# Performance work log

Hardware: AMD Instinct MI355X
Metric: run time of the kernel (lower is better)

## Reference

```python
import jax, jax.numpy as jnp
import numpy as np

B, C, Hf, Wf, HM, P = 64, 2048, 16, 16, 256, 10  # P = num_parts, NP = graph nodes
NP = P - 1
EPS = 1e-5  # BatchNorm eps

def bn_eval(x, g, b, rm, rv):
    return (x - rm) * jax.lax.rsqrt(rv + EPS) * g + b

def setup_inputs() -> dict:
    key = jax.random.key(0)
    ks = jax.random.split(key, 6)
    return {
        "x_global": jax.random.normal(ks[0], (B, C, Hf, Wf), jnp.float32),
        "x_gcn": jax.random.normal(ks[1], (B, C, Hf, Wf), jnp.float32),
        "mask": jax.random.randint(ks[2], (B, 1, HM, HM), 0, P, jnp.int32),
        "adj": jax.random.uniform(ks[3], (B, NP, NP), jnp.float32),
        "W1": jax.random.normal(ks[4], (C, C), jnp.float32) * 0.02,
        "b1": jnp.zeros((C,), jnp.float32),
        "g1": jnp.ones((NP * C,), jnp.float32), "be1": jnp.zeros((NP * C,), jnp.float32),
        "rm1": jnp.zeros((NP * C,), jnp.float32), "rv1": jnp.ones((NP * C,), jnp.float32),
        "W2": jax.random.normal(ks[5], (C, C), jnp.float32) * 0.02,
        "b2": jnp.zeros((C,), jnp.float32),
        "g2": jnp.ones((NP * C,), jnp.float32), "be2": jnp.zeros((NP * C,), jnp.float32),
        "rm2": jnp.zeros((NP * C,), jnp.float32), "rv2": jnp.ones((NP * C,), jnp.float32),
        "gb_g": jnp.ones((C,), jnp.float32), "gb_b": jnp.zeros((C,), jnp.float32),
        "gb_rm": jnp.zeros((C,), jnp.float32), "gb_rv": jnp.ones((C,), jnp.float32),
        "gn_g": jnp.ones((C,), jnp.float32), "gn_b": jnp.zeros((C,), jnp.float32),
        "gn_rm": jnp.zeros((C,), jnp.float32), "gn_rv": jnp.ones((C,), jnp.float32),
    }

def gc_layer(x, adj, Wt, bias, g, be, rm, rv):
    # GraphConvolution: matmul -> bmm(adj) -> bias -> BN over flattened (B, NP*C)
    s = jnp.einsum('bpc,cd->bpd', x, Wt)
    o = jnp.einsum('bpq,bqd->bpd', adj, s) + bias
    flat = o.reshape(o.shape[0], -1)
    return bn_eval(flat, g, be, rm, rv).reshape(o.shape)

def reference(x_global, x_gcn, mask, adj, W1, b1, g1, be1, rm1, rv1,
              W2, b2, g2, be2, rm2, rv2, gb_g, gb_b, gb_rm, gb_rv,
              gn_g, gn_b, gn_rm, gn_rv):
    # --- global branch: GAP + bottleneck BN (eval) ---
    feat_global = x_global.mean(axis=(2, 3))                      # (B, C)
    bnfeat_global = bn_eval(feat_global, gb_g, gb_b, gb_rm, gb_rv)

    # --- nearest-neighbor downsample of mask to feature-map size ---
    stride = HM // Hf
    mr = mask[:, 0, ::stride, ::stride]                           # (B, h, w)

    # one-hot part masks for classes 1..P-1: (B, h, w, NP)
    onehot = (mr[..., None] == jnp.arange(1, P)).astype(jnp.float32)
    counts = onehot.sum(axis=(1, 2))                              # (B, NP)

    # deterministic part dropout: drop the first present part per image
    drop = jnp.argmax(counts > 0, axis=1) + 1                     # (B,)
    keep = (mr != drop[:, None, None]).astype(jnp.float32)        # (B, h, w)
    x_self = x_gcn * keep[:, None, :, :]

    # segment mean pooling per part: (B, NP, C)
    denom = (counts + 1e-8)[..., None]
    mask_feat = jnp.einsum('bchw,bhwp->bpc', x_gcn, onehot) / denom
    self_feat = jnp.einsum('bchw,bhwp->bpc', x_self, onehot) / denom

    def gcn(x):
        x1 = jax.nn.relu(gc_layer(x, adj, W1, b1, g1, be1, rm1, rv1))
        x2 = jax.nn.relu(gc_layer(x1, adj, W2, b2, g2, be2, rm2, rv2))
        return x2.mean(axis=1), x2.reshape(x2.shape[0], -1)

    feat_gcn, feat_gcn_cat = gcn(mask_feat)
    feat_self, feat_self_cat = gcn(self_feat)
    bnfeat_gcn = bn_eval(feat_gcn, gn_g, gn_b, gn_rm, gn_rv)
    bnfeat_self = bn_eval(feat_self, gn_g, gn_b, gn_rm, gn_rv)

    # concatenate eval-mode outputs into one array: (B, 3*C + 2*NP*C)
    return jnp.concatenate([bnfeat_global, bnfeat_gcn, bnfeat_self,
                            feat_gcn_cat, feat_self_cat], axis=1)
```

## Files before the change

kernel.cpp:

```cpp
#include <hip/hip_runtime.h>
#include <cstdint>
#include <cstddef>

#define EPSV 1e-5f

typedef __bf16 bf16x8 __attribute__((ext_vector_type(8)));
typedef float f32x4 __attribute__((ext_vector_type(4)));

__device__ __forceinline__ unsigned short f2bf(float f) {
  unsigned int u = __float_as_uint(f);
  u += 0x7FFFu + ((u >> 16) & 1u);
  return (unsigned short)(u >> 16);
}

__device__ __forceinline__ void async_copy16(const void* src, void* dst_lds) {
  __builtin_amdgcn_global_load_lds(
      (const __attribute__((address_space(1))) void*)src,
      (__attribute__((address_space(3))) void*)dst_lds, 16, 0, 0);
}

__global__ __launch_bounds__(256) void kmean(
    const float* __restrict__ x, const float* __restrict__ g,
    const float* __restrict__ bb, const float* __restrict__ rm,
    const float* __restrict__ rv, float* __restrict__ out) {
  int gw = blockIdx.x * 4 + (threadIdx.x >> 6);
  int lane = threadIdx.x & 63;
  float4 v = ((const float4*)(x + (size_t)gw * 256))[lane];
  float s = v.x + v.y + v.z + v.w;
#pragma unroll
  for (int o = 32; o > 0; o >>= 1) s += __shfl_xor(s, o, 64);
  if (lane == 0) {
    int b = gw >> 11, c = gw & 2047;
    float m = s * (1.f / 256.f);
    out[(size_t)b * 43008 + c] =
        (m - rm[c]) / sqrtf(rv[c] + EPSV) * g[c] + bb[c];
  }
}

__global__ __launch_bounds__(256) void kmask(
    const int* __restrict__ mask, int* __restrict__ partid,
    float* __restrict__ invden, int* __restrict__ dropm1) {
  int b = blockIdx.x;
  int t = threadIdx.x;
  int h = t >> 4, w = t & 15;
  int m = mask[(size_t)b * 65536 + h * 4096 + w * 16];
  partid[b * 256 + t] = m;
  __shared__ int cnt[10];
  if (t < 10) cnt[t] = 0;
  __syncthreads();
  atomicAdd(&cnt[m], 1);
  __syncthreads();
  if (t == 0) {
    int dp = 0;
    for (int p = 8; p >= 0; p--)
      if (cnt[p + 1] > 0) dp = p;
    dropm1[b] = dp;
  }
  if (t < 9) invden[b * 9 + t] = 1.f / ((float)cnt[t + 1] + 1e-8f);
}

__global__ __launch_bounds__(256) void kpool(
    const float* __restrict__ x, const int* __restrict__ partid,
    const float* __restrict__ invden, const int* __restrict__ dropm1,
    unsigned short* __restrict__ Abuf) {
  int gw = blockIdx.x * 4 + (threadIdx.x >> 6);
  int lane = threadIdx.x & 63;
  int b = gw >> 11, c = gw & 2047;
  int4 pid = ((const int4*)(partid + b * 256))[lane];
  float4 v = ((const float4*)(x + (size_t)gw * 256))[lane];
  float acc[9];
#pragma unroll
  for (int p = 0; p < 9; p++) acc[p] = 0.f;
#pragma unroll
  for (int p = 0; p < 9; p++) {
    acc[p] += (pid.x == p + 1) ? v.x : 0.f;
    acc[p] += (pid.y == p + 1) ? v.y : 0.f;
    acc[p] += (pid.z == p + 1) ? v.z : 0.f;
    acc[p] += (pid.w == p + 1) ? v.w : 0.f;
  }
#pragma unroll
  for (int p = 0; p < 9; p++) {
    float s = acc[p];
#pragma unroll
    for (int o = 32; o > 0; o >>= 1) s += __shfl_xor(s, o, 64);
    acc[p] = s;
  }
  if (lane == 0) {
    int dm1 = dropm1[b];
#pragma unroll
    for (int p = 0; p < 9; p++) {
      float val = acc[p] * invden[b * 9 + p];
      unsigned short h = f2bf(val);
      Abuf[(size_t)(b * 9 + p) * 2048 + c] = h;
      Abuf[(size_t)((64 + b) * 9 + p) * 2048 + c] =
          (p == dm1) ? (unsigned short)0 : h;
    }
  }
}

__global__ __launch_bounds__(256) void ktranspose(
    const float* __restrict__ W, unsigned short* __restrict__ Wt) {
  __shared__ float tile[32][33];
  int tx = threadIdx.x & 31;
  int ty = threadIdx.x >> 5;
  int k0 = blockIdx.y * 32;
  int n0 = blockIdx.x * 32;
#pragma unroll
  for (int i = 0; i < 32; i += 8)
    tile[ty + i][tx] = W[(size_t)(k0 + ty + i) * 2048 + n0 + tx];
  __syncthreads();
#pragma unroll
  for (int i = 0; i < 32; i += 8)
    Wt[(size_t)(n0 + ty + i) * 2048 + k0 + tx] = f2bf(tile[tx][ty + i]);
}

#define GK 2048
__global__ __launch_bounds__(256) void gemm_bf16(
    const unsigned short* __restrict__ A, const unsigned short* __restrict__ Bt,
    float* __restrict__ S) {
  __shared__ unsigned short As[128 * 32];
  __shared__ unsigned short Bs[128 * 32];
  const int tid = threadIdx.x;
  const int lane = tid & 63;
  const int wave = tid >> 6;
  const int wm = (wave >> 1) << 6;
  const int wn = (wave & 1) << 6;
  const int quad = lane >> 4;
  const int l16 = lane & 15;
  const int by = blockIdx.y;
  const int bx = blockIdx.x;

  const unsigned short* Ag = A + (size_t)by * 128 * GK;
  const unsigned short* Bg = Bt + (size_t)bx * 128 * GK;

  f32x4 acc[4][4];
#pragma unroll
  for (int i = 0; i < 4; i++)
#pragma unroll
    for (int j = 0; j < 4; j++) acc[i][j] = (f32x4){0.f, 0.f, 0.f, 0.f};

  const int seg0 = tid, seg1 = tid + 256;
  const int r0 = seg0 >> 2, c0 = (seg0 & 3) * 8;
  const int r1 = seg1 >> 2, c1 = (seg1 & 3) * 8;

  for (int kk = 0; kk < GK; kk += 32) {
    __syncthreads();
    async_copy16(Ag + (size_t)r0 * GK + kk + c0, &As[seg0 * 8]);
    async_copy16(Ag + (size_t)r1 * GK + kk + c1, &As[seg1 * 8]);
    async_copy16(Bg + (size_t)r0 * GK + kk + c0, &Bs[seg0 * 8]);
    async_copy16(Bg + (size_t)r1 * GK + kk + c1, &Bs[seg1 * 8]);
    asm volatile("s_waitcnt vmcnt(0)" ::: "memory");
    __syncthreads();

    bf16x8 af[4], bfr[4];
#pragma unroll
    for (int i = 0; i < 4; i++)
      af[i] = *(const bf16x8*)&As[(wm + i * 16 + l16) * 32 + quad * 8];
#pragma unroll
    for (int j = 0; j < 4; j++)
      bfr[j] = *(const bf16x8*)&Bs[(wn + j * 16 + l16) * 32 + quad * 8];
#pragma unroll
    for (int i = 0; i < 4; i++)
#pragma unroll
      for (int j = 0; j < 4; j++)
        acc[i][j] = __builtin_amdgcn_mfma_f32_16x16x32_bf16(af[i], bfr[j],
                                                            acc[i][j], 0, 0, 0);
  }

#pragma unroll
  for (int i = 0; i < 4; i++)
#pragma unroll
    for (int j = 0; j < 4; j++)
#pragma unroll
      for (int r = 0; r < 4; r++) {
        int m = by * 128 + wm + i * 16 + quad * 4 + r;
        int n = bx * 128 + wn + j * 16 + l16;
        S[(size_t)m * 2048 + n] = acc[i][j][r];
      }
}

__global__ __launch_bounds__(256) void epi_mid(
    const float* __restrict__ S, const float* __restrict__ adj,
    const float* __restrict__ bias, const float* __restrict__ g,
    const float* __restrict__ be, const float* __restrict__ rm,
    const float* __restrict__ rv, unsigned short* __restrict__ Aout) {
  int idx = blockIdx.x * 256 + threadIdx.x;
  int d = idx & 2047;
  int bb = idx >> 11;
  int b = bb & 63;
  float s[9];
#pragma unroll
  for (int q = 0; q < 9; q++) s[q] = S[(size_t)(bb * 9 + q) * 2048 + d];
#pragma unroll
  for (int p = 0; p < 9; p++) {
    float o = bias[d];
#pragma unroll
    for (int q = 0; q < 9; q++) o += adj[b * 81 + p * 9 + q] * s[q];
    int f = p * 2048 + d;
    float v = (o - rm[f]) / sqrtf(rv[f] + EPSV) * g[f] + be[f];
    v = fmaxf(v, 0.f);
    Aout[(size_t)(bb * 9 + p) * 2048 + d] = f2bf(v);
  }
}

__global__ __launch_bounds__(256) void epi_final(
    const float* __restrict__ S, const float* __restrict__ adj,
    const float* __restrict__ bias, const float* __restrict__ g,
    const float* __restrict__ be, const float* __restrict__ rm,
    const float* __restrict__ rv, const float* __restrict__ gn_g,
    const float* __restrict__ gn_b, const float* __restrict__ gn_rm,
    const float* __restrict__ gn_rv, float* __restrict__ out) {
  int idx = blockIdx.x * 256 + threadIdx.x;
  int d = idx & 2047;
  int bb = idx >> 11;
  int b = bb & 63;
  bool selfb = bb >= 64;
  float s[9];
#pragma unroll
  for (int q = 0; q < 9; q++) s[q] = S[(size_t)(bb * 9 + q) * 2048 + d];
  float* orow = out + (size_t)b * 43008;
  size_t catbase = selfb ? 24576 : 6144;
  float mean = 0.f;
#pragma unroll
  for (int p = 0; p < 9; p++) {
    float o = bias[d];
#pragma unroll
    for (int q = 0; q < 9; q++) o += adj[b * 81 + p * 9 + q] * s[q];
    int f = p * 2048 + d;
    float v = (o - rm[f]) / sqrtf(rv[f] + EPSV) * g[f] + be[f];
    v = fmaxf(v, 0.f);
    mean += v;
    orow[catbase + f] = v;
  }
  mean *= (1.f / 9.f);
  orow[(selfb ? 4096 : 2048) + d] =
      (mean - gn_rm[d]) / sqrtf(gn_rv[d] + EPSV) * gn_g[d] + gn_b[d];
}

extern "C" void kernel_launch(void* const* d_in, const int* in_sizes, int n_in,
                              void* d_out, int out_size, void* d_ws,
                              size_t ws_size, hipStream_t stream) {
  const float* x_global = (const float*)d_in[0];
  const float* x_gcn = (const float*)d_in[1];
  const int* mask = (const int*)d_in[2];
  const float* adj = (const float*)d_in[3];
  const float* W1 = (const float*)d_in[4];
  const float* b1 = (const float*)d_in[5];
  const float* g1 = (const float*)d_in[6];
  const float* be1 = (const float*)d_in[7];
  const float* rm1 = (const float*)d_in[8];
  const float* rv1 = (const float*)d_in[9];
  const float* W2 = (const float*)d_in[10];
  const float* b2 = (const float*)d_in[11];
  const float* g2 = (const float*)d_in[12];
  const float* be2 = (const float*)d_in[13];
  const float* rm2 = (const float*)d_in[14];
  const float* rv2 = (const float*)d_in[15];
  const float* gb_g = (const float*)d_in[16];
  const float* gb_b = (const float*)d_in[17];
  const float* gb_rm = (const float*)d_in[18];
  const float* gb_rv = (const float*)d_in[19];
  const float* gn_g = (const float*)d_in[20];
  const float* gn_b = (const float*)d_in[21];
  const float* gn_rm = (const float*)d_in[22];
  const float* gn_rv = (const float*)d_in[23];
  float* out = (float*)d_out;

  char* ws = (char*)d_ws;
  int* partid = (int*)(ws);
  float* invden = (float*)(ws + 65536);
  int* dropm1 = (int*)(ws + 67840);
  unsigned short* Abuf = (unsigned short*)(ws + 131072);
  unsigned short* Wt1 = (unsigned short*)(ws + 131072 + 4718592);
  unsigned short* Wt2 =
      (unsigned short*)(ws + 131072 + 4718592 + 8388608);
  float* S = (float*)(ws + 131072 + 4718592 + 2 * 8388608);

  ktranspose<<<dim3(64, 64), 256, 0, stream>>>(W1, Wt1);
  ktranspose<<<dim3(64, 64), 256, 0, stream>>>(W2, Wt2);
  kmean<<<32768, 256, 0, stream>>>(x_global, gb_g, gb_b, gb_rm, gb_rv, out);
  kmask<<<64, 256, 0, stream>>>(mask, partid, invden, dropm1);
  kpool<<<32768, 256, 0, stream>>>(x_gcn, partid, invden, dropm1, Abuf);
  gemm_bf16<<<dim3(16, 9), 256, 0, stream>>>(Abuf, Wt1, S);
  epi_mid<<<1024, 256, 0, stream>>>(S, adj, b1, g1, be1, rm1, rv1, Abuf);
  gemm_bf16<<<dim3(16, 9), 256, 0, stream>>>(Abuf, Wt2, S);
  epi_final<<<1024, 256, 0, stream>>>(S, adj, b2, g2, be2, rm2, rv2, gn_g,
                                      gn_b, gn_rm, gn_rv, out);
}
```

Before: 504.0 us.

## Use MFMA for part pooling, split-K the GCN GEMMs, merge weight transposes

Part pooling now runs as a bf16 MFMA matmul. Each block turns 64 channels of x into bf16 in LDS and multiplies them by a one-hot part matrix, replacing the per-channel wave shuffle reductions across 32768 blocks. The two 1152x2048x2048 GEMMs use a split-K of 2 to double the grid from 144 blocks. The epilogues sum the two partial result buffers. The two weight-transpose launches become one launch. The trade-offs are rounding x to bf16 before the reduction instead of after, an extra S buffer of workspace plus the epilogue reads for it, and the launch overhead of the larger grid.

```diff
diff --git a/kernel.cpp b/kernel.cpp
--- a/kernel.cpp
+++ b/kernel.cpp
@@ -59,47 +59,71 @@
   if (t < 9) invden[b * 9 + t] = 1.f / ((float)cnt[t + 1] + 1e-8f);
 }
 
-__global__ __launch_bounds__(256) void kpool(
+__global__ __launch_bounds__(256) void kpool_mfma(
     const float* __restrict__ x, const int* __restrict__ partid,
     const float* __restrict__ invden, const int* __restrict__ dropm1,
     unsigned short* __restrict__ Abuf) {
-  int gw = blockIdx.x * 4 + (threadIdx.x >> 6);
-  int lane = threadIdx.x & 63;
-  int b = gw >> 11, c = gw & 2047;
-  int4 pid = ((const int4*)(partid + b * 256))[lane];
-  float4 v = ((const float4*)(x + (size_t)gw * 256))[lane];
-  float acc[9];
-#pragma unroll
-  for (int p = 0; p < 9; p++) acc[p] = 0.f;
-#pragma unroll
-  for (int p = 0; p < 9; p++) {
-    acc[p] += (pid.x == p + 1) ? v.x : 0.f;
-    acc[p] += (pid.y == p + 1) ? v.y : 0.f;
-    acc[p] += (pid.z == p + 1) ? v.z : 0.f;
-    acc[p] += (pid.w == p + 1) ? v.w : 0.f;
-  }
-#pragma unroll
-  for (int p = 0; p < 9; p++) {
-    float s = acc[p];
-#pragma unroll
-    for (int o = 32; o > 0; o >>= 1) s += __shfl_xor(s, o, 64);
-    acc[p] = s;
-  }
-  if (lane == 0) {
+  __shared__ unsigned short As[64 * 264];
+  __shared__ unsigned short Bs[16 * 264];
+  __shared__ int pid[256];
+  const int t = threadIdx.x;
+  const int b = blockIdx.y;
+  const int c0 = blockIdx.x * 64;
+
+  pid[t] = partid[b * 256 + t];
+
+  const float4* xg = (const float4*)(x + ((size_t)(b * 2048 + c0)) * 256);
+#pragma unroll
+  for (int it = 0; it < 16; it++) {
+    int idx = t + it * 256;
+    float4 v = xg[idx];
+    int row = idx >> 6, sc = (idx & 63) * 4;
+    ushort4 h;
+    h.x = f2bf(v.x); h.y = f2bf(v.y); h.z = f2bf(v.z); h.w = f2bf(v.w);
+    *(ushort4*)&As[row * 264 + sc] = h;
+  }
+  __syncthreads();
+  {
+    int p = t >> 4, s0 = (t & 15) * 16;
+#pragma unroll
+    for (int j = 0; j < 16; j++)
+      Bs[p * 264 + s0 + j] =
+          (pid[s0 + j] == p + 1) ? (unsigned short)0x3F80 : (unsigned short)0;
+  }
+  __syncthreads();
+
+  const int wave = t >> 6;
+  const int l16 = t & 15;
+  const int quad = (t & 63) >> 4;
+  f32x4 acc = (f32x4){0.f, 0.f, 0.f, 0.f};
+#pragma unroll
+  for (int ks = 0; ks < 8; ks++) {
+    bf16x8 a = *(const bf16x8*)&As[(wave * 16 + l16) * 264 + ks * 32 + quad * 8];
+    bf16x8 bf = *(const bf16x8*)&Bs[l16 * 264 + ks * 32 + quad * 8];
+    acc = __builtin_amdgcn_mfma_f32_16x16x32_bf16(a, bf, acc, 0, 0, 0);
+  }
+
+  if (l16 < 9) {
+    int p = l16;
+    float inv = invden[b * 9 + p];
     int dm1 = dropm1[b];
-#pragma unroll
-    for (int p = 0; p < 9; p++) {
-      float val = acc[p] * invden[b * 9 + p];
-      unsigned short h = f2bf(val);
-      Abuf[(size_t)(b * 9 + p) * 2048 + c] = h;
-      Abuf[(size_t)((64 + b) * 9 + p) * 2048 + c] =
-          (p == dm1) ? (unsigned short)0 : h;
-    }
+    int cbase = c0 + wave * 16 + quad * 4;
+    ushort4 hm;
+    hm.x = f2bf(acc[0] * inv);
+    hm.y = f2bf(acc[1] * inv);
+    hm.z = f2bf(acc[2] * inv);
+    hm.w = f2bf(acc[3] * inv);
+    ushort4 hs = (p == dm1) ? (ushort4){0, 0, 0, 0} : hm;
+    *(ushort4*)&Abuf[(size_t)(b * 9 + p) * 2048 + cbase] = hm;
+    *(ushort4*)&Abuf[(size_t)((64 + b) * 9 + p) * 2048 + cbase] = hs;
   }
 }
 
 __global__ __launch_bounds__(256) void ktranspose(
-    const float* __restrict__ W, unsigned short* __restrict__ Wt) {
+    const float* __restrict__ W1, const float* __restrict__ W2,
+    unsigned short* __restrict__ Wt1, unsigned short* __restrict__ Wt2) {
+  const float* W = blockIdx.z ? W2 : W1;
+  unsigned short* Wt = blockIdx.z ? Wt2 : Wt1;
   __shared__ float tile[32][33];
   int tx = threadIdx.x & 31;
   int ty = threadIdx.x >> 5;
@@ -129,9 +153,11 @@
   const int l16 = lane & 15;
   const int by = blockIdx.y;
   const int bx = blockIdx.x;
+  const int kz = blockIdx.z;
 
   const unsigned short* Ag = A + (size_t)by * 128 * GK;
   const unsigned short* Bg = Bt + (size_t)bx * 128 * GK;
+  S += (size_t)kz * 1152 * 2048;
 
   f32x4 acc[4][4];
 #pragma unroll
@@ -143,7 +169,8 @@
   const int r0 = seg0 >> 2, c0 = (seg0 & 3) * 8;
   const int r1 = seg1 >> 2, c1 = (seg1 & 3) * 8;
 
-  for (int kk = 0; kk < GK; kk += 32) {
+  const int kbeg = kz * (GK / 2), kend = kbeg + (GK / 2);
+  for (int kk = kbeg; kk < kend; kk += 32) {
     __syncthreads();
     async_copy16(Ag + (size_t)r0 * GK + kk + c0, &As[seg0 * 8]);
     async_copy16(Ag + (size_t)r1 * GK + kk + c1, &As[seg1 * 8]);
@@ -180,17 +207,21 @@
 }
 
 __global__ __launch_bounds__(256) void epi_mid(
-    const float* __restrict__ S, const float* __restrict__ adj,
-    const float* __restrict__ bias, const float* __restrict__ g,
-    const float* __restrict__ be, const float* __restrict__ rm,
-    const float* __restrict__ rv, unsigned short* __restrict__ Aout) {
+    const float* __restrict__ S0, const float* __restrict__ S1,
+    const float* __restrict__ adj, const float* __restrict__ bias,
+    const float* __restrict__ g, const float* __restrict__ be,
+    const float* __restrict__ rm, const float* __restrict__ rv,
+    unsigned short* __restrict__ Aout) {
   int idx = blockIdx.x * 256 + threadIdx.x;
   int d = idx & 2047;
   int bb = idx >> 11;
   int b = bb & 63;
   float s[9];
 #pragma unroll
-  for (int q = 0; q < 9; q++) s[q] = S[(size_t)(bb * 9 + q) * 2048 + d];
+  for (int q = 0; q < 9; q++) {
+    size_t off = (size_t)(bb * 9 + q) * 2048 + d;
+    s[q] = S0[off] + S1[off];
+  }
 #pragma unroll
   for (int p = 0; p < 9; p++) {
     float o = bias[d];
@@ -204,12 +235,13 @@
 }
 
 __global__ __launch_bounds__(256) void epi_final(
-    const float* __restrict__ S, const float* __restrict__ adj,
-    const float* __restrict__ bias, const float* __restrict__ g,
-    const float* __restrict__ be, const float* __restrict__ rm,
-    const float* __restrict__ rv, const float* __restrict__ gn_g,
-    const float* __restrict__ gn_b, const float* __restrict__ gn_rm,
-    const float* __restrict__ gn_rv, float* __restrict__ out) {
+    const float* __restrict__ S0, const float* __restrict__ S1,
+    const float* __restrict__ adj, const float* __restrict__ bias,
+    const float* __restrict__ g, const float* __restrict__ be,
+    const float* __restrict__ rm, const float* __restrict__ rv,
+    const float* __restrict__ gn_g, const float* __restrict__ gn_b,
+    const float* __restrict__ gn_rm, const float* __restrict__ gn_rv,
+    float* __restrict__ out) {
   int idx = blockIdx.x * 256 + threadIdx.x;
   int d = idx & 2047;
   int bb = idx >> 11;
@@ -217,7 +249,10 @@
   bool selfb = bb >= 64;
   float s[9];
 #pragma unroll
-  for (int q = 0; q < 9; q++) s[q] = S[(size_t)(bb * 9 + q) * 2048 + d];
+  for (int q = 0; q < 9; q++) {
+    size_t off = (size_t)(bb * 9 + q) * 2048 + d;
+    s[q] = S0[off] + S1[off];
+  }
   float* orow = out + (size_t)b * 43008;
   size_t catbase = selfb ? 24576 : 6144;
   float mean = 0.f;
@@ -274,16 +309,17 @@
   unsigned short* Wt1 = (unsigned short*)(ws + 131072 + 4718592);
   unsigned short* Wt2 =
       (unsigned short*)(ws + 131072 + 4718592 + 8388608);
-  float* S = (float*)(ws + 131072 + 4718592 + 2 * 8388608);
-
-  ktranspose<<<dim3(64, 64), 256, 0, stream>>>(W1, Wt1);
-  ktranspose<<<dim3(64, 64), 256, 0, stream>>>(W2, Wt2);
+  float* S0 = (float*)(ws + 131072 + 4718592 + 2 * 8388608);
+  float* S1 = S0 + (size_t)1152 * 2048;
+
+  ktranspose<<<dim3(64, 64, 2), 256, 0, stream>>>(W1, W2, Wt1, Wt2);
   kmean<<<32768, 256, 0, stream>>>(x_global, gb_g, gb_b, gb_rm, gb_rv, out);
   kmask<<<64, 256, 0, stream>>>(mask, partid, invden, dropm1);
-  kpool<<<32768, 256, 0, stream>>>(x_gcn, partid, invden, dropm1, Abuf);
-  gemm_bf16<<<dim3(16, 9), 256, 0, stream>>>(Abuf, Wt1, S);
-  epi_mid<<<1024, 256, 0, stream>>>(S, adj, b1, g1, be1, rm1, rv1, Abuf);
-  gemm_bf16<<<dim3(16, 9), 256, 0, stream>>>(Abuf, Wt2, S);
-  epi_final<<<1024, 256, 0, stream>>>(S, adj, b2, g2, be2, rm2, rv2, gn_g,
+  kpool_mfma<<<dim3(32, 64), 256, 0, stream>>>(x_gcn, partid, invden, dropm1,
+                                               Abuf);
+  gemm_bf16<<<dim3(16, 9, 2), 256, 0, stream>>>(Abuf, Wt1, S0);
+  epi_mid<<<1024, 256, 0, stream>>>(S0, S1, adj, b1, g1, be1, rm1, rv1, Abuf);
+  gemm_bf16<<<dim3(16, 9, 2), 256, 0, stream>>>(Abuf, Wt2, S0);
+  epi_final<<<1024, 256, 0, stream>>>(S0, S1, adj, b2, g2, be2, rm2, rv2, gn_g,
                                       gn_b, gn_rm, gn_rv, out);
 }
```

Result: faster. 429.5 us (-14.8%).
